# Optimization experiments

Hardware: AMD Instinct MI355X
Metric: run time of the kernel (lower is better)

## Reference

```python
import jax, jax.numpy as jnp
import numpy as np

NETS = 32
NODES = [256, 512, 512, 128]
BATCH = 4096


def setup_inputs() -> dict:
    key = jax.random.key(0)
    ks = jax.random.split(key, 7)
    def lin_init(k, n_out, n_in):
        # mimic nn.Linear default init scale
        bound = 1.0 / np.sqrt(n_in)
        kw, kb = jax.random.split(k)
        W = jax.random.uniform(kw, (NETS, n_out, n_in), jnp.float32, -bound, bound)
        b = jax.random.uniform(kb, (NETS, n_out), jnp.float32, -bound, bound)
        return W, b
    x = jax.random.normal(ks[0], (BATCH, NODES[0]), jnp.float32)
    W1, b1 = lin_init(ks[1], NODES[1], NODES[0])
    W2, b2 = lin_init(ks[2], NODES[2], NODES[1])
    W3, b3 = lin_init(ks[3], NODES[3], NODES[2])
    return {"x": x, "W1": W1, "b1": b1, "W2": W2, "b2": b2, "W3": W3, "b3": b3}


def reference(x, W1, b1, W2, b2, W3, b3):
    # Ensemble of independent MLPs expressed as batched GEMMs over the `nets` axis.
    # x: [B, in]; Wl: [N, out_l, in_l]; bl: [N, out_l]
    h = jax.nn.relu(jnp.einsum('bi,noi->bno', x, W1) + b1)        # [B, N, 512]
    h = jax.nn.relu(jnp.einsum('bni,noi->bno', h, W2) + b2)       # [B, N, 512]
    out = jnp.einsum('bni,noi->bno', h, W3) + b3                  # [B, N, 128] (identity act)
    B = x.shape[0]
    # Concatenate per-net outputs along feature dim: y[:, n*out_len:(n+1)*out_len]
    return out.reshape(B, -1)
```

## Files before the change

kernel.cpp:

```cpp
#include <hip/hip_runtime.h>

#define NETS 32
#define BATCH 4096
#define D0 256
#define D1 512
#define D2 512
#define D3 128
#define MT 64
#define LDA (D0 + 8)
#define LDH (D1 + 8)

using half8 = __attribute__((ext_vector_type(8))) _Float16;
using half4 = __attribute__((ext_vector_type(4))) _Float16;
using f32x4 = __attribute__((ext_vector_type(4))) float;

#define W1_N (NETS * D1 * D0)
#define W2_N (NETS * D2 * D1)
#define W3_N (NETS * D3 * D2)

template<int N, int K, int NI, int NWCH>
__device__ __forceinline__ void cvt_one(const float* __restrict__ W, _Float16* __restrict__ Wh, int u) {
    constexpr int NF = (K / 32) * NI;
    const int p = u & 31;
    const int f = u >> 5;
    const int fn = f % NF;
    const int netw = f / NF;
    const int kk = fn / NI, ni = fn % NI;
    const int net = netw >> 2, w = netw & 3;
    const int r = p & 15;
    const int kh = (p >> 4) * 16;
    const int n = w * NWCH + ni * 16 + r;
    const float* src = W + (size_t)net * N * K + (size_t)n * K + kk * 32 + kh;
    float4 v0 = *reinterpret_cast<const float4*>(src);
    float4 v1 = *reinterpret_cast<const float4*>(src + 4);
    float4 v2 = *reinterpret_cast<const float4*>(src + 8);
    float4 v3 = *reinterpret_cast<const float4*>(src + 12);
    half8 o0, o1;
    o0[0] = (_Float16)v0.x; o0[1] = (_Float16)v0.y; o0[2] = (_Float16)v0.z; o0[3] = (_Float16)v0.w;
    o0[4] = (_Float16)v1.x; o0[5] = (_Float16)v1.y; o0[6] = (_Float16)v1.z; o0[7] = (_Float16)v1.w;
    o1[0] = (_Float16)v2.x; o1[1] = (_Float16)v2.y; o1[2] = (_Float16)v2.z; o1[3] = (_Float16)v2.w;
    o1[4] = (_Float16)v3.x; o1[5] = (_Float16)v3.y; o1[6] = (_Float16)v3.z; o1[7] = (_Float16)v3.w;
    const int l1 = (kh >> 3) * 16 + r;
    _Float16* dst = Wh + (size_t)f * 512 + l1 * 8;
    *reinterpret_cast<half8*>(dst) = o0;
    *reinterpret_cast<half8*>(dst + 128) = o1;
}

__global__ void cvt_weights(const float* __restrict__ W1, const float* __restrict__ W2,
                            const float* __restrict__ W3,
                            _Float16* __restrict__ W1h, _Float16* __restrict__ W2h,
                            _Float16* __restrict__ W3h) {
    const int i = blockIdx.x * blockDim.x + threadIdx.x;
    constexpr int T1 = W1_N / 16, T2 = W2_N / 16;
    if (i < T1)            cvt_one<D1, D0, 8, 128>(W1, W1h, i);
    else if (i < T1 + T2)  cvt_one<D2, D1, 8, 128>(W2, W2h, i - T1);
    else                   cvt_one<D3, D2, 2,  32>(W3, W3h, i - T1 - T2);
}

template<int K, int NI, int MI, int D>
__device__ __forceinline__ void layer_mfma(const _Float16* As, int lda,
                                           const _Float16* __restrict__ wl,
                                           int lane16, int quad,
                                           f32x4 (&acc)[MI][NI]) {
    constexpr int NKK = K / 32;
    half8 b[D + 1][NI];
#pragma unroll
    for (int d = 0; d < D; ++d)
#pragma unroll
        for (int ni = 0; ni < NI; ++ni)
            b[d][ni] = *reinterpret_cast<const half8*>(wl + (size_t)(d * NI + ni) * 512);
#pragma unroll
    for (int kk = 0; kk < NKK; ++kk) {
        if (kk + D < NKK) {
            const int slot = (kk + D) % (D + 1);
#pragma unroll
            for (int ni = 0; ni < NI; ++ni)
                b[slot][ni] = *reinterpret_cast<const half8*>(
                    wl + (size_t)((kk + D) * NI + ni) * 512);
        }
        half8 a[MI];
#pragma unroll
        for (int mi = 0; mi < MI; ++mi)
            a[mi] = *reinterpret_cast<const half8*>(
                As + (mi * 16 + lane16) * lda + kk * 32 + quad * 8);
        const int cs = kk % (D + 1);
#pragma unroll
        for (int ni = 0; ni < NI; ++ni)
#pragma unroll
            for (int mi = 0; mi < MI; ++mi)
                acc[mi][ni] = __builtin_amdgcn_mfma_f32_16x16x32_f16(a[mi], b[cs][ni], acc[mi][ni], 0, 0, 0);
    }
}

template<int MI, int NI>
__device__ __forceinline__ void store_act(f32x4 (&acc)[MI][NI], const float* __restrict__ bias,
                                          _Float16* dst, int ldd, int n_base,
                                          int lane16, int quad) {
#pragma unroll
    for (int ni = 0; ni < NI; ++ni) {
        float bv = bias[n_base + ni * 16 + lane16];
        int col = n_base + ni * 16 + lane16;
#pragma unroll
        for (int mi = 0; mi < MI; ++mi) {
#pragma unroll
            for (int r = 0; r < 4; ++r) {
                float v = acc[mi][ni][r] + bv;
                v = fmaxf(v, 0.0f);
                int row = mi * 16 + quad * 4 + r;
                dst[row * ldd + col] = (_Float16)v;
            }
        }
    }
}

__global__ __launch_bounds__(256, 2) void mlp_fused(
    const float* __restrict__ X,
    const _Float16* __restrict__ W1h, const float* __restrict__ b1,
    const _Float16* __restrict__ W2h, const float* __restrict__ b2,
    const _Float16* __restrict__ W3h, const float* __restrict__ b3,
    float* __restrict__ out) {
    __shared__ __align__(16) _Float16 buf[MT * LDH];

    const int tid = threadIdx.x;
    const int w = tid >> 6;
    const int l = tid & 63;
    const int lane16 = l & 15;
    const int quad = l >> 4;

    const int bb = blockIdx.x;
    const int xcd = bb & 7;
    const int s = bb >> 3;
    const int net = xcd * 4 + (s >> 6);
    const int mt = s & 63;
    const int m0 = mt * MT;

    {
        const float* xsrc = X + (size_t)m0 * D0;
#pragma unroll
        for (int it = 0; it < 16; ++it) {
            int chunk = it * 256 + tid;
            int row = chunk >> 6;
            int c4 = chunk & 63;
            float4 v = *reinterpret_cast<const float4*>(xsrc + row * D0 + c4 * 4);
            half4 o;
            o[0] = (_Float16)v.x; o[1] = (_Float16)v.y;
            o[2] = (_Float16)v.z; o[3] = (_Float16)v.w;
            *reinterpret_cast<half4*>(&buf[row * LDA + c4 * 4]) = o;
        }
    }
    __syncthreads();

    {
        f32x4 acc[4][8] = {};
        const _Float16* wl = W1h + ((size_t)(net * 4 + w) * 64) * 512 + l * 8;
        layer_mfma<D0, 8, 4, 1>(buf, LDA, wl, lane16, quad, acc);
        __syncthreads();
        store_act<4, 8>(acc, b1 + net * D1, buf, LDH, w * 128, lane16, quad);
    }
    __syncthreads();

    {
        f32x4 acc[4][8] = {};
        const _Float16* wl = W2h + ((size_t)(net * 4 + w) * 128) * 512 + l * 8;
        layer_mfma<D1, 8, 4, 1>(buf, LDH, wl, lane16, quad, acc);
        __syncthreads();
        store_act<4, 8>(acc, b2 + net * D2, buf, LDH, w * 128, lane16, quad);
    }
    __syncthreads();

    {
        f32x4 acc[4][2] = {};
        const _Float16* wl = W3h + ((size_t)(net * 4 + w) * 32) * 512 + l * 8;
        layer_mfma<D2, 2, 4, 3>(buf, LDH, wl, lane16, quad, acc);
        const int n_base = w * 32;
#pragma unroll
        for (int ni = 0; ni < 2; ++ni) {
            float bv = b3[net * D3 + n_base + ni * 16 + lane16];
            int col = net * D3 + n_base + ni * 16 + lane16;
#pragma unroll
            for (int mi = 0; mi < 4; ++mi) {
#pragma unroll
                for (int r = 0; r < 4; ++r) {
                    int row = m0 + mi * 16 + quad * 4 + r;
                    out[(size_t)row * (NETS * D3) + col] = acc[mi][ni][r] + bv;
                }
            }
        }
    }
}

extern "C" void kernel_launch(void* const* d_in, const int* in_sizes, int n_in,
                              void* d_out, int out_size, void* d_ws, size_t ws_size,
                              hipStream_t stream) {
    const float* x  = (const float*)d_in[0];
    const float* W1 = (const float*)d_in[1];
    const float* b1 = (const float*)d_in[2];
    const float* W2 = (const float*)d_in[3];
    const float* b2 = (const float*)d_in[4];
    const float* W3 = (const float*)d_in[5];
    const float* b3 = (const float*)d_in[6];
    float* out = (float*)d_out;

    _Float16* W1h = (_Float16*)d_ws;
    _Float16* W2h = W1h + (size_t)W1_N;
    _Float16* W3h = W2h + (size_t)W2_N;

    const int totalT = (W1_N + W2_N + W3_N) / 16;
    cvt_weights<<<totalT / 256, 256, 0, stream>>>(W1, W2, W3, W1h, W2h, W3h);

    mlp_fused<<<NETS * (BATCH / MT), 256, 0, stream>>>(x, W1h, b1, W2h, b2, W3h, b3, out);
}
```

Measured before the change: 247.7 us.

## Switch to 32x32x16 MFMA tiles and pre-convert input to fp16

Replaces the 16x16x32 MFMA tiling with 32x32x16 MFMA, re-laying out the pre-packed fp16 weight fragments and the accumulator-to-row mapping to match. Larger MFMA tiles mean fewer LDS A-fragment loads per FLOP and fewer instructions. The input x is also converted to fp16 once in the pre-pass kernel instead of in every block (each x tile was being reconverted by all 32 nets). This adds an extra global fp16 copy of x and a deeper weight prefetch for layer 3, which raises register pressure.

```diff
diff --git a/kernel.cpp b/kernel.cpp
--- a/kernel.cpp
+++ b/kernel.cpp
@@ -10,27 +10,25 @@
 #define LDA (D0 + 8)
 #define LDH (D1 + 8)
 
-using half8 = __attribute__((ext_vector_type(8))) _Float16;
-using half4 = __attribute__((ext_vector_type(4))) _Float16;
-using f32x4 = __attribute__((ext_vector_type(4))) float;
+using half8  = __attribute__((ext_vector_type(8))) _Float16;
+using f32x16 = __attribute__((ext_vector_type(16))) float;
 
 #define W1_N (NETS * D1 * D0)
 #define W2_N (NETS * D2 * D1)
 #define W3_N (NETS * D3 * D2)
-
-template<int N, int K, int NI, int NWCH>
-__device__ __forceinline__ void cvt_one(const float* __restrict__ W, _Float16* __restrict__ Wh, int u) {
-    constexpr int NF = (K / 32) * NI;
-    const int p = u & 31;
-    const int f = u >> 5;
-    const int fn = f % NF;
-    const int netw = f / NF;
-    const int kk = fn / NI, ni = fn % NI;
-    const int net = netw >> 2, w = netw & 3;
-    const int r = p & 15;
-    const int kh = (p >> 4) * 16;
-    const int n = w * NWCH + ni * 16 + r;
-    const float* src = W + (size_t)net * N * K + (size_t)n * K + kk * 32 + kh;
+#define X_N  (BATCH * D0)
+
+template<int N, int K, int NI, int WSH>
+__device__ __forceinline__ void cvt_w(const float* __restrict__ W, _Float16* __restrict__ Wh, int u) {
+    constexpr int NKK = K / 16;
+    const int t  = u % NKK;
+    const int rg = u / NKK;
+    const int n   = rg % N;
+    const int net = rg / N;
+    const int w  = n >> WSH;
+    const int ni = (n >> 5) & (NI - 1);
+    const int m  = n & 31;
+    const float* src = W + (size_t)net * N * K + (size_t)n * K + t * 16;
     float4 v0 = *reinterpret_cast<const float4*>(src);
     float4 v1 = *reinterpret_cast<const float4*>(src + 4);
     float4 v2 = *reinterpret_cast<const float4*>(src + 8);
@@ -40,29 +38,46 @@
     o0[4] = (_Float16)v1.x; o0[5] = (_Float16)v1.y; o0[6] = (_Float16)v1.z; o0[7] = (_Float16)v1.w;
     o1[0] = (_Float16)v2.x; o1[1] = (_Float16)v2.y; o1[2] = (_Float16)v2.z; o1[3] = (_Float16)v2.w;
     o1[4] = (_Float16)v3.x; o1[5] = (_Float16)v3.y; o1[6] = (_Float16)v3.z; o1[7] = (_Float16)v3.w;
-    const int l1 = (kh >> 3) * 16 + r;
-    _Float16* dst = Wh + (size_t)f * 512 + l1 * 8;
-    *reinterpret_cast<half8*>(dst) = o0;
-    *reinterpret_cast<half8*>(dst + 128) = o1;
-}
-
-__global__ void cvt_weights(const float* __restrict__ W1, const float* __restrict__ W2,
-                            const float* __restrict__ W3,
-                            _Float16* __restrict__ W1h, _Float16* __restrict__ W2h,
-                            _Float16* __restrict__ W3h) {
+    const int f = ((net * 4 + w) * NKK + t) * NI + ni;
+    _Float16* dst = Wh + (size_t)f * 512 + m * 8;
+    *reinterpret_cast<half8*>(dst)       = o0;
+    *reinterpret_cast<half8*>(dst + 256) = o1;
+}
+
+__global__ void cvt_all(const float* __restrict__ x,
+                        const float* __restrict__ W1, const float* __restrict__ W2,
+                        const float* __restrict__ W3,
+                        _Float16* __restrict__ Xh,
+                        _Float16* __restrict__ W1h, _Float16* __restrict__ W2h,
+                        _Float16* __restrict__ W3h) {
     const int i = blockIdx.x * blockDim.x + threadIdx.x;
-    constexpr int T1 = W1_N / 16, T2 = W2_N / 16;
-    if (i < T1)            cvt_one<D1, D0, 8, 128>(W1, W1h, i);
-    else if (i < T1 + T2)  cvt_one<D2, D1, 8, 128>(W2, W2h, i - T1);
-    else                   cvt_one<D3, D2, 2,  32>(W3, W3h, i - T1 - T2);
+    constexpr int TX = X_N / 16, T1 = W1_N / 16, T2 = W2_N / 16;
+    if (i < TX) {
+        const float* src = x + (size_t)i * 16;
+        float4 v0 = *reinterpret_cast<const float4*>(src);
+        float4 v1 = *reinterpret_cast<const float4*>(src + 4);
+        float4 v2 = *reinterpret_cast<const float4*>(src + 8);
+        float4 v3 = *reinterpret_cast<const float4*>(src + 12);
+        half8 o0, o1;
+        o0[0] = (_Float16)v0.x; o0[1] = (_Float16)v0.y; o0[2] = (_Float16)v0.z; o0[3] = (_Float16)v0.w;
+        o0[4] = (_Float16)v1.x; o0[5] = (_Float16)v1.y; o0[6] = (_Float16)v1.z; o0[7] = (_Float16)v1.w;
+        o1[0] = (_Float16)v2.x; o1[1] = (_Float16)v2.y; o1[2] = (_Float16)v2.z; o1[3] = (_Float16)v2.w;
+        o1[4] = (_Float16)v3.x; o1[5] = (_Float16)v3.y; o1[6] = (_Float16)v3.z; o1[7] = (_Float16)v3.w;
+        _Float16* dst = Xh + (size_t)i * 16;
+        *reinterpret_cast<half8*>(dst)     = o0;
+        *reinterpret_cast<half8*>(dst + 8) = o1;
+    }
+    else if (i < TX + T1)           cvt_w<D1, D0, 4, 7>(W1, W1h, i - TX);
+    else if (i < TX + T1 + T2)      cvt_w<D2, D1, 4, 7>(W2, W2h, i - TX - T1);
+    else                            cvt_w<D3, D2, 1, 5>(W3, W3h, i - TX - T1 - T2);
 }
 
 template<int K, int NI, int MI, int D>
-__device__ __forceinline__ void layer_mfma(const _Float16* As, int lda,
-                                           const _Float16* __restrict__ wl,
-                                           int lane16, int quad,
-                                           f32x4 (&acc)[MI][NI]) {
-    constexpr int NKK = K / 32;
+__device__ __forceinline__ void layer32(const _Float16* As, int lda,
+                                        const _Float16* __restrict__ wl,
+                                        int lane_m, int oct,
+                                        f32x16 (&acc)[MI][NI]) {
+    constexpr int NKK = K / 16;
     half8 b[D + 1][NI];
 #pragma unroll
     for (int d = 0; d < D; ++d)
@@ -82,31 +97,31 @@
 #pragma unroll
         for (int mi = 0; mi < MI; ++mi)
             a[mi] = *reinterpret_cast<const half8*>(
-                As + (mi * 16 + lane16) * lda + kk * 32 + quad * 8);
+                As + (mi * 32 + lane_m) * lda + kk * 16 + oct * 8);
         const int cs = kk % (D + 1);
 #pragma unroll
         for (int ni = 0; ni < NI; ++ni)
 #pragma unroll
             for (int mi = 0; mi < MI; ++mi)
-                acc[mi][ni] = __builtin_amdgcn_mfma_f32_16x16x32_f16(a[mi], b[cs][ni], acc[mi][ni], 0, 0, 0);
+                acc[mi][ni] = __builtin_amdgcn_mfma_f32_32x32x16_f16(a[mi], b[cs][ni], acc[mi][ni], 0, 0, 0);
     }
 }
 
 template<int MI, int NI>
-__device__ __forceinline__ void store_act(f32x4 (&acc)[MI][NI], const float* __restrict__ bias,
-                                          _Float16* dst, int ldd, int n_base,
-                                          int lane16, int quad) {
+__device__ __forceinline__ void store_act32(f32x16 (&acc)[MI][NI], const float* __restrict__ bias,
+                                            _Float16* dst, int ldd, int n_base,
+                                            int lane_m, int oct) {
 #pragma unroll
     for (int ni = 0; ni < NI; ++ni) {
-        float bv = bias[n_base + ni * 16 + lane16];
-        int col = n_base + ni * 16 + lane16;
+        const int col = n_base + ni * 32 + lane_m;
+        float bv = bias[col];
 #pragma unroll
         for (int mi = 0; mi < MI; ++mi) {
 #pragma unroll
-            for (int r = 0; r < 4; ++r) {
+            for (int r = 0; r < 16; ++r) {
                 float v = acc[mi][ni][r] + bv;
                 v = fmaxf(v, 0.0f);
-                int row = mi * 16 + quad * 4 + r;
+                int row = mi * 32 + (r & 3) + 8 * (r >> 2) + 4 * oct;
                 dst[row * ldd + col] = (_Float16)v;
             }
         }
@@ -114,7 +129,7 @@
 }
 
 __global__ __launch_bounds__(256, 2) void mlp_fused(
-    const float* __restrict__ X,
+    const _Float16* __restrict__ Xh,
     const _Float16* __restrict__ W1h, const float* __restrict__ b1,
     const _Float16* __restrict__ W2h, const float* __restrict__ b2,
     const _Float16* __restrict__ W3h, const float* __restrict__ b3,
@@ -124,8 +139,8 @@
     const int tid = threadIdx.x;
     const int w = tid >> 6;
     const int l = tid & 63;
-    const int lane16 = l & 15;
-    const int quad = l >> 4;
+    const int lane_m = l & 31;
+    const int oct = l >> 5;
 
     const int bb = blockIdx.x;
     const int xcd = bb & 7;
@@ -135,55 +150,48 @@
     const int m0 = mt * MT;
 
     {
-        const float* xsrc = X + (size_t)m0 * D0;
-#pragma unroll
-        for (int it = 0; it < 16; ++it) {
+        const _Float16* xsrc = Xh + (size_t)m0 * D0;
+#pragma unroll
+        for (int it = 0; it < 8; ++it) {
             int chunk = it * 256 + tid;
-            int row = chunk >> 6;
-            int c4 = chunk & 63;
-            float4 v = *reinterpret_cast<const float4*>(xsrc + row * D0 + c4 * 4);
-            half4 o;
-            o[0] = (_Float16)v.x; o[1] = (_Float16)v.y;
-            o[2] = (_Float16)v.z; o[3] = (_Float16)v.w;
-            *reinterpret_cast<half4*>(&buf[row * LDA + c4 * 4]) = o;
+            int row = chunk >> 5;
+            int c8 = chunk & 31;
+            *reinterpret_cast<half8*>(&buf[row * LDA + c8 * 8]) =
+                *reinterpret_cast<const half8*>(xsrc + row * D0 + c8 * 8);
         }
     }
     __syncthreads();
 
     {
-        f32x4 acc[4][8] = {};
+        f32x16 acc[2][4] = {};
         const _Float16* wl = W1h + ((size_t)(net * 4 + w) * 64) * 512 + l * 8;
-        layer_mfma<D0, 8, 4, 1>(buf, LDA, wl, lane16, quad, acc);
+        layer32<D0, 4, 2, 2>(buf, LDA, wl, lane_m, oct, acc);
         __syncthreads();
-        store_act<4, 8>(acc, b1 + net * D1, buf, LDH, w * 128, lane16, quad);
+        store_act32<2, 4>(acc, b1 + net * D1, buf, LDH, w * 128, lane_m, oct);
     }
     __syncthreads();
 
     {
-        f32x4 acc[4][8] = {};
+        f32x16 acc[2][4] = {};
         const _Float16* wl = W2h + ((size_t)(net * 4 + w) * 128) * 512 + l * 8;
-        layer_mfma<D1, 8, 4, 1>(buf, LDH, wl, lane16, quad, acc);
+        layer32<D1, 4, 2, 2>(buf, LDH, wl, lane_m, oct, acc);
         __syncthreads();
-        store_act<4, 8>(acc, b2 + net * D2, buf, LDH, w * 128, lane16, quad);
+        store_act32<2, 4>(acc, b2 + net * D2, buf, LDH, w * 128, lane_m, oct);
     }
     __syncthreads();
 
     {
-        f32x4 acc[4][2] = {};
+        f32x16 acc[2][1] = {};
         const _Float16* wl = W3h + ((size_t)(net * 4 + w) * 32) * 512 + l * 8;
-        layer_mfma<D2, 2, 4, 3>(buf, LDH, wl, lane16, quad, acc);
-        const int n_base = w * 32;
-#pragma unroll
-        for (int ni = 0; ni < 2; ++ni) {
-            float bv = b3[net * D3 + n_base + ni * 16 + lane16];
-            int col = net * D3 + n_base + ni * 16 + lane16;
-#pragma unroll
-            for (int mi = 0; mi < 4; ++mi) {
-#pragma unroll
-                for (int r = 0; r < 4; ++r) {
-                    int row = m0 + mi * 16 + quad * 4 + r;
-                    out[(size_t)row * (NETS * D3) + col] = acc[mi][ni][r] + bv;
-                }
+        layer32<D2, 1, 2, 8>(buf, LDH, wl, lane_m, oct, acc);
+        const int col = net * D3 + w * 32 + lane_m;
+        float bv = b3[net * D3 + w * 32 + lane_m];
+#pragma unroll
+        for (int mi = 0; mi < 2; ++mi) {
+#pragma unroll
+            for (int r = 0; r < 16; ++r) {
+                int row = m0 + mi * 32 + (r & 3) + 8 * (r >> 2) + 4 * oct;
+                out[(size_t)row * (NETS * D3) + col] = acc[mi][0][r] + bv;
             }
         }
     }
@@ -201,12 +209,13 @@
     const float* b3 = (const float*)d_in[6];
     float* out = (float*)d_out;
 
-    _Float16* W1h = (_Float16*)d_ws;
+    _Float16* Xh  = (_Float16*)d_ws;
+    _Float16* W1h = Xh  + (size_t)X_N;
     _Float16* W2h = W1h + (size_t)W1_N;
     _Float16* W3h = W2h + (size_t)W2_N;
 
-    const int totalT = (W1_N + W2_N + W3_N) / 16;
-    cvt_weights<<<totalT / 256, 256, 0, stream>>>(W1, W2, W3, W1h, W2h, W3h);
-
-    mlp_fused<<<NETS * (BATCH / MT), 256, 0, stream>>>(x, W1h, b1, W2h, b2, W3h, b3, out);
-}
+    const int totalT = (X_N + W1_N + W2_N + W3_N) / 16;
+    cvt_all<<<totalT / 256, 256, 0, stream>>>(x, W1, W2, W3, Xh, W1h, W2h, W3h);
+
+    mlp_fused<<<NETS * (BATCH / MT), 256, 0, stream>>>(Xh, W1h, b1, W2h, b2, W3h, b3, out);
+}
```

New measurement: 244.7 us. About the same (-1.2%).
